# Performance work log

Measured on AMD Instinct MI355X. Metric: run time of the kernel, lower is better.

## Reference

```python
import jax, jax.numpy as jnp
import numpy as np

B_IN, C_OUT, K, P, STRIDE, ITERS = 32, 32, 3, 4, 2, 3
PSIZE = P * P
EPS = 1e-08
LAMBDA = 0.001
LN_2PI = float(np.log(2.0 * np.pi))


def _patch(t, K, stride):
    # t: (b, h, w, B, d) -> (b, oh, ow, K, K, B, d)
    b, h, w, B, d = t.shape
    oh = (h - K + 1) // stride
    idxs = jnp.arange(oh)[:, None] * stride + jnp.arange(K)[None, :]  # (oh, K)
    t = t[:, idxs]            # (b, oh, K, w, B, d)
    t = t[:, :, :, idxs]      # (b, oh, K, ow, K, B, d)
    t = jnp.transpose(t, (0, 1, 3, 2, 4, 5, 6))  # (b, oh, ow, K, K, B, d)
    return t, oh, oh


def _em_routing(v, a_in, beta_u, beta_a):
    # v: (b,h,w,Bn,C,psize); a_in: (b,h,w,Bn,1)
    b, h, w, Bn, C, psize = v.shape
    mu = sigma_sq = a_out = None
    for it in range(ITERS):
        if it == 0:
            r = jnp.full((b, h, w, Bn, C), 1.0 / C, dtype=v.dtype) * a_in
        else:
            ln_pjh = -((v - mu) ** 2) / (2.0 * sigma_sq) - 0.5 * jnp.log(sigma_sq) - 0.5 * LN_2PI
            ln_ap = ln_pjh.sum(axis=5) + jnp.log(a_out.reshape(b, h, w, 1, C))
            r = jax.nn.softmax(ln_ap, axis=4)
        r_sum = r.sum(axis=3, keepdims=True)                 # (b,h,w,1,C)
        coeff = (r / (r_sum + EPS))[..., None]               # (b,h,w,Bn,C,1)
        mu = jnp.sum(coeff * v, axis=3, keepdims=True)       # (b,h,w,1,C,psize)
        sigma_sq = jnp.sum(coeff * (v - mu) ** 2, axis=3, keepdims=True)
        r_sum6 = r_sum[..., None]                            # (b,h,w,1,C,1)
        cost_h = (beta_u + 0.5 * jnp.log(sigma_sq)) * r_sum6 # log(sqrt(s)) = 0.5*log(s)
        a_out = jax.nn.sigmoid(LAMBDA * (beta_a - cost_h.sum(axis=5, keepdims=True)))
    return mu.reshape(b, h, w, C, psize), a_out.reshape(b, h, w, C, 1)


def setup_inputs() -> dict:
    key = jax.random.key(0)
    k1, k2, k3 = jax.random.split(key, 3)
    b, h, w = 16, 14, 14
    x = jax.random.normal(k1, (b, h, w, B_IN, PSIZE), dtype=jnp.float32)
    a = jax.random.uniform(k2, (b, h, w, B_IN, 1), dtype=jnp.float32)
    weights = jax.random.normal(k3, (1, 1, 1, K * K * B_IN, C_OUT, P, P), dtype=jnp.float32)
    beta_u = jnp.zeros((C_OUT, 1), dtype=jnp.float32)
    beta_a = jnp.zeros((C_OUT, 1), dtype=jnp.float32)
    return {"x": x, "a": a, "weights": weights, "beta_u": beta_u, "beta_a": beta_a}


def reference(x, a, weights, beta_u, beta_a):
    b = x.shape[0]
    p_in, oh, ow = _patch(x, K, STRIDE)
    a_in, _, _ = _patch(a, K, STRIDE)
    KKB = K * K * B_IN
    p_in = p_in.reshape(b, oh, ow, KKB, PSIZE)
    a_in = a_in.reshape(b, oh, ow, KKB, 1)
    # voting: per-capsule PxP pose matmul with transformation matrices
    pose = p_in.reshape(b, oh, ow, KKB, P, P)
    W = weights.reshape(KKB, C_OUT, P, P)
    v = jnp.einsum('bhwnij,ncjl->bhwncil', pose, W).reshape(b, oh, ow, KKB, C_OUT, PSIZE)
    return _em_routing(v, a_in, beta_u, beta_a)
```

## Files before the change

### kernel.cpp

```cpp
#include <hip/hip_runtime.h>


#define LN2PI 1.8378770664093453f
#define LOG2E 1.4426950408889634f

typedef __attribute__((ext_vector_type(2))) float f32x2;
#define FMA2(a, b, c) __builtin_elementwise_fma((a), (b), (c))
__device__ __forceinline__ f32x2 splat2(float x) { f32x2 r; r.x = x; r.y = x; return r; }

#define DPP_ADD(x, ctrl) \
    ((x) + __int_as_float(__builtin_amdgcn_update_dpp( \
        0, __float_as_int(x), (ctrl), 0xF, 0xF, true)))

__device__ __forceinline__ float sum32(float e) {
    float s = e;
    s = DPP_ADD(s, 0xB1);
    s = DPP_ADD(s, 0x4E);
    s = DPP_ADD(s, 0x141);
    s = DPP_ADD(s, 0x140);
    s += __shfl_xor(s, 16);
    return s;
}

__global__ __launch_bounds__(256)
void wtrans(const float4* __restrict__ W4, float4* __restrict__ Wt)
{
    int idx = blockIdx.x * 256 + threadIdx.x;
    if (idx < 36864) {
        int n = idx >> 7;
        int r = idx & 127;
        int c = r >> 2, q = r & 3;
        Wt[((n * 4 + q) << 5) + c] = W4[idx];
    }
}

__global__ __launch_bounds__(256, 2)
void em_fused(const float* __restrict__ x,
              const float* __restrict__ a,
              const float4* __restrict__ Wt,
              const float* __restrict__ bu,
              const float* __restrict__ ba,
              float* __restrict__ out)
{
    __shared__ __align__(16) float4 pose_s[288 * 4];
    __shared__ float ain_s[288];
    __shared__ float SA[2][32][17];
    __shared__ float SB[2][32][17];
    __shared__ f32x2 php_s[32][9];
    __shared__ f32x2 mh_s[32][9];
    __shared__ float A_s[32];
    __shared__ float AU_s[32];

    const int tid  = threadIdx.x;
    const int wv   = tid >> 6;
    const int lane = tid & 63;
    const int half = (lane >> 5) & 1;
    const int c    = lane & 31;

    const int pos = blockIdx.x;
    const int b   = pos / 36;
    const int rem = pos % 36;
    const int oy  = rem / 6, ox = rem % 6;
    const int iy0 = oy * 2, ix0 = ox * 2;

    {
        const float4* x4 = (const float4*)x;
        for (int idx = tid; idx < 1152; idx += 256) {
            int seg = idx >> 7, u = idx & 127;
            int kh = seg / 3, kw = seg % 3;
            pose_s[idx] = x4[((b * 14 + iy0 + kh) * 14 + (ix0 + kw)) * 128 + u];
        }
        for (int idx = tid; idx < 288; idx += 256) {
            int seg = idx >> 5, bi = idx & 31;
            int kh = seg / 3, kw = seg % 3;
            ain_s[idx] = a[((b * 14 + iy0 + kh) * 14 + (ix0 + kw)) * 32 + bi] * 0.03125f;
        }
    }
    __syncthreads();

    const int n0 = wv * 72 + half;

    for (int it = 0; it < 3; ++it) {
        f32x2 ph[8], mh[8];
        float Ac = 0.f;
        if (it > 0) {
            #pragma unroll
            for (int j = 0; j < 8; ++j) { ph[j] = php_s[c][j]; mh[j] = mh_s[c][j]; }
            float AU = AU_s[c];
            float m = AU;
            #pragma unroll
            for (int mk = 16; mk >= 1; mk >>= 1)
                m = fmaxf(m, __shfl_xor(m, mk));
            Ac = A_s[c] - m;
        }

        f32x2 s1[8], s2[8];
        #pragma unroll
        for (int j = 0; j < 8; ++j) { s1[j] = splat2(0.f); s2[j] = splat2(0.f); }
        float Racc = 0.f;

        const float4* wp = Wt + (size_t)n0 * 128 + c;
        const float4* pp = pose_s + n0 * 4;
        const float* an  = ain_s + n0;

        for (int s = 0; s < 18; ++s) {
            float4 wa0 = wp[0],   wa1 = wp[32],  wa2 = wp[64],  wa3 = wp[96];
            float4 wb0 = wp[256], wb1 = wp[288], wb2 = wp[320], wb3 = wp[352];
            float4 pa0 = pp[0],  pa1 = pp[1],  pa2 = pp[2],  pa3 = pp[3];
            float4 pb0 = pp[8],  pb1 = pp[9],  pb2 = pp[10], pb3 = pp[11];

            f32x2 wa[8], wb[8];
            wa[0].x=wa0.x; wa[0].y=wa0.y;  wa[1].x=wa0.z; wa[1].y=wa0.w;
            wa[2].x=wa1.x; wa[2].y=wa1.y;  wa[3].x=wa1.z; wa[3].y=wa1.w;
            wa[4].x=wa2.x; wa[4].y=wa2.y;  wa[5].x=wa2.z; wa[5].y=wa2.w;
            wa[6].x=wa3.x; wa[6].y=wa3.y;  wa[7].x=wa3.z; wa[7].y=wa3.w;
            wb[0].x=wb0.x; wb[0].y=wb0.y;  wb[1].x=wb0.z; wb[1].y=wb0.w;
            wb[2].x=wb1.x; wb[2].y=wb1.y;  wb[3].x=wb1.z; wb[3].y=wb1.w;
            wb[4].x=wb2.x; wb[4].y=wb2.y;  wb[5].x=wb2.z; wb[5].y=wb2.w;
            wb[6].x=wb3.x; wb[6].y=wb3.y;  wb[7].x=wb3.z; wb[7].y=wb3.w;

            f32x2 va[8], vb[8];
            #pragma unroll
            for (int i = 0; i < 4; ++i) {
                float4 pra = (i == 0) ? pa0 : (i == 1) ? pa1 : (i == 2) ? pa2 : pa3;
                float4 prb = (i == 0) ? pb0 : (i == 1) ? pb1 : (i == 2) ? pb2 : pb3;
                #pragma unroll
                for (int lp = 0; lp < 2; ++lp) {
                    f32x2 ta = splat2(pra.x) * wa[0 + lp];
                    f32x2 tb = splat2(prb.x) * wb[0 + lp];
                    ta = FMA2(splat2(pra.y), wa[2 + lp], ta);
                    tb = FMA2(splat2(prb.y), wb[2 + lp], tb);
                    ta = FMA2(splat2(pra.z), wa[4 + lp], ta);
                    tb = FMA2(splat2(prb.z), wb[4 + lp], tb);
                    ta = FMA2(splat2(pra.w), wa[6 + lp], ta);
                    tb = FMA2(splat2(prb.w), wb[6 + lp], tb);
                    va[i * 2 + lp] = ta;
                    vb[i * 2 + lp] = tb;
                }
            }

            float ra, rb;
            if (it == 0) {
                ra = an[4 * s];
                rb = an[4 * s + 2];
            } else {
                f32x2 aa = splat2(0.f), ab = splat2(0.f);
                aa.x = Ac; ab.x = Ac;
                #pragma unroll
                for (int j = 0; j < 8; ++j) {
                    f32x2 ta = FMA2(ph[j], va[j], mh[j]);
                    f32x2 tb = FMA2(ph[j], vb[j], mh[j]);
                    aa = FMA2(ta, va[j], aa);
                    ab = FMA2(tb, vb[j], ab);
                }
                float ea = __builtin_amdgcn_exp2f(aa.x + aa.y);
                float eb = __builtin_amdgcn_exp2f(ab.x + ab.y);
                float sa = sum32(ea);
                float sb = sum32(eb);
                ra = __fdividef(ea, sa + 1e-30f);
                rb = __fdividef(eb, sb + 1e-30f);
            }

            Racc += ra + rb;
            f32x2 rra = splat2(ra), rrb = splat2(rb);
            #pragma unroll
            for (int j = 0; j < 8; ++j) {
                f32x2 rva = rra * va[j];
                f32x2 rvb = rrb * vb[j];
                s1[j] = s1[j] + rva + rvb;
                s2[j] = FMA2(rva, va[j], s2[j]);
                s2[j] = FMA2(rvb, vb[j], s2[j]);
            }

            wp += 512;
            pp += 16;
        }

        #pragma unroll
        for (int j = 0; j < 8; ++j) {
            s1[j].x += __shfl_xor(s1[j].x, 32);
            s1[j].y += __shfl_xor(s1[j].y, 32);
            s2[j].x += __shfl_xor(s2[j].x, 32);
            s2[j].y += __shfl_xor(s2[j].y, 32);
        }
        Racc += __shfl_xor(Racc, 32);

        if (wv >= 2) {
            const int row = wv - 2;
            if (half == 0) {
                #pragma unroll
                for (int j = 0; j < 8; ++j) {
                    SA[row][c][2 * j]     = s1[j].x;
                    SA[row][c][2 * j + 1] = s1[j].y;
                }
                SA[row][c][16] = Racc;
            } else {
                #pragma unroll
                for (int j = 0; j < 8; ++j) {
                    SB[row][c][2 * j]     = s2[j].x;
                    SB[row][c][2 * j + 1] = s2[j].y;
                }
            }
        }
        __syncthreads();
        if (wv < 2) {
            if (half == 0) {
                #pragma unroll
                for (int j = 0; j < 8; ++j) {
                    SA[wv][c][2 * j]     += s1[j].x;
                    SA[wv][c][2 * j + 1] += s1[j].y;
                }
                SA[wv][c][16] += Racc;
            } else {
                #pragma unroll
                for (int j = 0; j < 8; ++j) {
                    SB[wv][c][2 * j]     += s2[j].x;
                    SB[wv][c][2 * j + 1] += s2[j].y;
                }
            }
        }
        __syncthreads();

        {
            const int cf = tid >> 3, k2 = tid & 7;
            float R = SA[0][cf][16] + SA[1][cf][16];
            float rinv = __fdividef(1.f, R + 1e-8f);
            float muv[2];
            float tpart = 0.f, Ks = 0.f;
            #pragma unroll
            for (int t2 = 0; t2 < 2; ++t2) {
                int k = k2 + t2 * 8;
                float sv1 = SA[0][cf][k] + SA[1][cf][k];
                float sv2 = SB[0][cf][k] + SB[1][cf][k];
                float mu  = sv1 * rinv;
                float sig = fmaf(-mu, mu, sv2 * rinv);
                sig = fmaxf(sig, 1e-30f);
                float p = __fdividef(0.5f, sig);
                muv[t2] = mu;
                if (it < 2) {
                    ((float*)&php_s[cf][0])[k] = -p * LOG2E;
                    ((float*)&mh_s[cf][0])[k]  = 2.f * p * mu * LOG2E;
                }
                tpart += __logf(sig);
                Ks = fmaf(p * mu, mu, Ks);
            }
            #pragma unroll
            for (int mk = 4; mk >= 1; mk >>= 1) {
                tpart += __shfl_xor(tpart, mk);
                Ks    += __shfl_xor(Ks, mk);
            }
            float cost = R * fmaf(0.5f, tpart, 16.f * bu[cf]);
            float aout = __fdividef(1.f, 1.f + __expf(-(0.001f * (ba[cf] - cost))));

            if (it < 2) {
                if (k2 == 0) {
                    float Afold = __logf(aout) - 0.5f * tpart - 8.0f * LN2PI - Ks;
                    A_s[cf]  = Afold * LOG2E;
                    AU_s[cf] = (Afold + Ks) * LOG2E;
                }
            } else {
                out[(size_t)pos * 512 + cf * 16 + k2]     = muv[0];
                out[(size_t)pos * 512 + cf * 16 + k2 + 8] = muv[1];
                if (k2 == 0)
                    out[294912 + pos * 32 + cf] = aout;
            }
        }
        __syncthreads();
    }
}

#define NB 288
#define LNSTEP 36
__global__ __launch_bounds__(256, 2)
void convcaps_em_legacy(const float* __restrict__ x, const float* __restrict__ a,
                        const float* __restrict__ W, const float* __restrict__ bu,
                        const float* __restrict__ ba, float* __restrict__ out)
{
    __shared__ __align__(16) float pose_s[NB * 16];
    __shared__ __align__(16) float ain_s[NB];
    __shared__ float S1w[4][32][17];
    __shared__ float S2w[4][32][17];
    __shared__ float Rw[4][32];
    __shared__ float mu_s[32][17];
    __shared__ float p_s[32][17];
    __shared__ float A_s[32];

    const int tid = threadIdx.x, wv = tid >> 6, lane = tid & 63;
    const int half = (lane >> 5) & 1, c = lane & 31;
    const int bid = blockIdx.x, b = bid / 36, rem = bid % 36;
    const int oy = rem / 6, ox = rem % 6, iy0 = oy * 2, ix0 = ox * 2;
    {
        const float4* x4 = (const float4*)x;
        float4* d4 = (float4*)pose_s;
        for (int idx = tid; idx < 1152; idx += 256) {
            int seg = idx >> 7, u = idx & 127, kh = seg / 3, kw = seg % 3;
            d4[idx] = x4[((b * 14 + iy0 + kh) * 14 + (ix0 + kw)) * 128 + u];
        }
        const float4* a4 = (const float4*)a;
        float4* e4 = (float4*)ain_s;
        if (tid < 72) {
            int seg = tid >> 3, u = tid & 7, kh = seg / 3, kw = seg % 3;
            e4[tid] = a4[((b * 14 + iy0 + kh) * 14 + (ix0 + kw)) * 8 + u];
        }
    }
    __syncthreads();
    const float4* W4 = (const float4*)W;
    float muh[16], ph[16], Ac = 0.0f;
    #pragma unroll
    for (int i = 0; i < 16; ++i) { muh[i] = 0.0f; ph[i] = 0.0f; }
    for (int iter = 0; iter < 3; ++iter) {
        if (iter > 0) {
            #pragma unroll
            for (int il = 0; il < 16; ++il) { muh[il] = mu_s[c][il]; ph[il] = p_s[c][il]; }
            Ac = A_s[c];
        }
        float S1[16], S2[16], Racc = 0.0f;
        #pragma unroll
        for (int i = 0; i < 16; ++i) { S1[i] = 0.0f; S2[i] = 0.0f; }
        for (int s = 0; s < LNSTEP; ++s) {
            const int n = wv * 72 + 2 * s + half;
            float wreg[16], preg[16];
            const float4* wp = W4 + (size_t)(n * 32 + c) * 4;
            float4 w0 = wp[0], w1 = wp[1], w2 = wp[2], w3 = wp[3];
            wreg[0]=w0.x; wreg[1]=w0.y; wreg[2]=w0.z; wreg[3]=w0.w;
            wreg[4]=w1.x; wreg[5]=w1.y; wreg[6]=w1.z; wreg[7]=w1.w;
            wreg[8]=w2.x; wreg[9]=w2.y; wreg[10]=w2.z; wreg[11]=w2.w;
            wreg[12]=w3.x; wreg[13]=w3.y; wreg[14]=w3.z; wreg[15]=w3.w;
            const float4* pp = (const float4*)&pose_s[n * 16];
            float4 p0 = pp[0], p1 = pp[1], p2 = pp[2], p3 = pp[3];
            preg[0]=p0.x; preg[1]=p0.y; preg[2]=p0.z; preg[3]=p0.w;
            preg[4]=p1.x; preg[5]=p1.y; preg[6]=p1.z; preg[7]=p1.w;
            preg[8]=p2.x; preg[9]=p2.y; preg[10]=p2.z; preg[11]=p2.w;
            preg[12]=p3.x; preg[13]=p3.y; preg[14]=p3.z; preg[15]=p3.w;
            float v[16];
            #pragma unroll
            for (int i = 0; i < 4; ++i)
                #pragma unroll
                for (int l = 0; l < 4; ++l) {
                    float acc = preg[i*4+0] * wreg[l];
                    acc = fmaf(preg[i*4+1], wreg[4+l], acc);
                    acc = fmaf(preg[i*4+2], wreg[8+l], acc);
                    acc = fmaf(preg[i*4+3], wreg[12+l], acc);
                    v[i*4+l] = acc;
                }
            float r;
            if (iter == 0) r = ain_s[n] * 0.03125f;
            else {
                float acc = 0.0f;
                #pragma unroll
                for (int il = 0; il < 16; ++il) { float d = v[il]-muh[il]; acc = fmaf(-ph[il], d*d, acc); }
                float lnap = Ac + acc, m = lnap;
                #pragma unroll
                for (int mk = 16; mk >= 1; mk >>= 1) m = fmaxf(m, __shfl_xor(m, mk));
                float e = __expf(lnap - m), ssum = e;
                #pragma unroll
                for (int mk = 16; mk >= 1; mk >>= 1) ssum += __shfl_xor(ssum, mk);
                r = __fdividef(e, ssum);
            }
            Racc += r;
            #pragma unroll
            for (int il = 0; il < 16; ++il) { float rv = r * v[il]; S1[il] += rv; S2[il] = fmaf(rv, v[il], S2[il]); }
        }
        #pragma unroll
        for (int il = 0; il < 16; ++il) { S1[il] += __shfl_xor(S1[il], 32); S2[il] += __shfl_xor(S2[il], 32); }
        Racc += __shfl_xor(Racc, 32);
        if (half == 0) {
            #pragma unroll
            for (int il = 0; il < 16; ++il) { S1w[wv][c][il] = S1[il]; S2w[wv][c][il] = S2[il]; }
            Rw[wv][c] = Racc;
        }
        __syncthreads();
        {
            const int c2 = tid >> 3, k = tid & 7;
            float R = Rw[0][c2] + Rw[1][c2] + Rw[2][c2] + Rw[3][c2];
            float rinv = __fdividef(1.0f, R + 1e-8f);
            float muv[2], pv[2], tpart = 0.0f;
            #pragma unroll
            for (int t2 = 0; t2 < 2; ++t2) {
                int il = k + t2 * 8;
                float s1 = S1w[0][c2][il]+S1w[1][c2][il]+S1w[2][c2][il]+S1w[3][c2][il];
                float s2 = S2w[0][c2][il]+S2w[1][c2][il]+S2w[2][c2][il]+S2w[3][c2][il];
                float mu = s1 * rinv;
                float sig = fmaf(-mu, mu, s2 * rinv);
                sig = fmaxf(sig, 1e-30f);
                muv[t2] = mu; pv[t2] = __fdividef(0.5f, sig); tpart += __logf(sig);
            }
            #pragma unroll
            for (int mk = 4; mk >= 1; mk >>= 1) tpart += __shfl_xor(tpart, mk);
            float cost = R * fmaf(0.5f, tpart, 16.0f * bu[c2]);
            float aout = __fdividef(1.0f, 1.0f + __expf(-(0.001f * (ba[c2] - cost))));
            if (iter < 2) {
                #pragma unroll
                for (int t2 = 0; t2 < 2; ++t2) { int il = k + t2*8; mu_s[c2][il] = muv[t2]; p_s[c2][il] = pv[t2]; }
                if (k == 0) A_s[c2] = __logf(aout) - 0.5f * tpart - 8.0f * LN2PI;
            } else {
                #pragma unroll
                for (int t2 = 0; t2 < 2; ++t2) { int il = k + t2*8; out[(size_t)bid*512 + c2*16 + il] = muv[t2]; }
                if (k == 0) out[294912 + bid * 32 + c2] = aout;
            }
        }
        __syncthreads();
    }
}

extern "C" void kernel_launch(void* const* d_in, const int* in_sizes, int n_in,
                              void* d_out, int out_size, void* d_ws, size_t ws_size,
                              hipStream_t stream) {
    (void)in_sizes; (void)n_in; (void)out_size;
    const float* x  = (const float*)d_in[0];
    const float* a  = (const float*)d_in[1];
    const float* w  = (const float*)d_in[2];
    const float* bu = (const float*)d_in[3];
    const float* ba = (const float*)d_in[4];
    float* out = (float*)d_out;
    float* wsf = (float*)d_ws;

    if (ws_size >= (size_t)147456 * 4) {
        float* Wt = wsf;
        hipLaunchKernelGGL(wtrans, dim3(144), dim3(256), 0, stream,
                           (const float4*)w, (float4*)Wt);
        hipLaunchKernelGGL(em_fused, dim3(576), dim3(256), 0, stream,
                           x, a, (const float4*)Wt, bu, ba, out);
    } else {
        hipLaunchKernelGGL(convcaps_em_legacy, dim3(576), dim3(256), 0, stream,
                           x, a, w, bu, ba, out);
    }
}
```

Measured before the change: 92.76 us.

## Read pose directly from global memory and process one capsule per loop step

Drops the shared-memory staging of the pose patch. Each lane now loads its pose rows straight from global memory, with the address recomputed whenever the input capsule index crosses a 32-capsule segment. The inner loop handles one input capsule per iteration instead of two interleaved ones, and the occupancy hint is removed from launch_bounds. This removes the staging loads, the LDS traffic and part of the register pressure. In exchange the pose rows are re-read from global/L2 in every routing iteration and there is less instruction-level parallelism per loop step.

```diff
diff --git a/kernel.cpp b/kernel.cpp
--- a/kernel.cpp
+++ b/kernel.cpp
@@ -34,7 +34,7 @@
     }
 }
 
-__global__ __launch_bounds__(256, 2)
+__global__ __launch_bounds__(256)
 void em_fused(const float* __restrict__ x,
               const float* __restrict__ a,
               const float4* __restrict__ Wt,
@@ -42,7 +42,6 @@
               const float* __restrict__ ba,
               float* __restrict__ out)
 {
-    __shared__ __align__(16) float4 pose_s[288 * 4];
     __shared__ float ain_s[288];
     __shared__ float SA[2][32][17];
     __shared__ float SB[2][32][17];
@@ -63,18 +62,12 @@
     const int oy  = rem / 6, ox = rem % 6;
     const int iy0 = oy * 2, ix0 = ox * 2;
 
-    {
-        const float4* x4 = (const float4*)x;
-        for (int idx = tid; idx < 1152; idx += 256) {
-            int seg = idx >> 7, u = idx & 127;
-            int kh = seg / 3, kw = seg % 3;
-            pose_s[idx] = x4[((b * 14 + iy0 + kh) * 14 + (ix0 + kw)) * 128 + u];
-        }
-        for (int idx = tid; idx < 288; idx += 256) {
-            int seg = idx >> 5, bi = idx & 31;
-            int kh = seg / 3, kw = seg % 3;
-            ain_s[idx] = a[((b * 14 + iy0 + kh) * 14 + (ix0 + kw)) * 32 + bi] * 0.03125f;
-        }
+    const float4* x4 = (const float4*)x;
+
+    for (int idx = tid; idx < 288; idx += 256) {
+        int seg = idx >> 5, bi = idx & 31;
+        int kh = seg / 3, kw = seg % 3;
+        ain_s[idx] = a[((b * 14 + iy0 + kh) * 14 + (ix0 + kw)) * 32 + bi] * 0.03125f;
     }
     __syncthreads();
 
@@ -100,80 +93,76 @@
         float Racc = 0.f;
 
         const float4* wp = Wt + (size_t)n0 * 128 + c;
-        const float4* pp = pose_s + n0 * 4;
         const float* an  = ain_s + n0;
 
-        for (int s = 0; s < 18; ++s) {
-            float4 wa0 = wp[0],   wa1 = wp[32],  wa2 = wp[64],  wa3 = wp[96];
-            float4 wb0 = wp[256], wb1 = wp[288], wb2 = wp[320], wb3 = wp[352];
-            float4 pa0 = pp[0],  pa1 = pp[1],  pa2 = pp[2],  pa3 = pp[3];
-            float4 pb0 = pp[8],  pb1 = pp[9],  pb2 = pp[10], pb3 = pp[11];
-
-            f32x2 wa[8], wb[8];
-            wa[0].x=wa0.x; wa[0].y=wa0.y;  wa[1].x=wa0.z; wa[1].y=wa0.w;
-            wa[2].x=wa1.x; wa[2].y=wa1.y;  wa[3].x=wa1.z; wa[3].y=wa1.w;
-            wa[4].x=wa2.x; wa[4].y=wa2.y;  wa[5].x=wa2.z; wa[5].y=wa2.w;
-            wa[6].x=wa3.x; wa[6].y=wa3.y;  wa[7].x=wa3.z; wa[7].y=wa3.w;
-            wb[0].x=wb0.x; wb[0].y=wb0.y;  wb[1].x=wb0.z; wb[1].y=wb0.w;
-            wb[2].x=wb1.x; wb[2].y=wb1.y;  wb[3].x=wb1.z; wb[3].y=wb1.w;
-            wb[4].x=wb2.x; wb[4].y=wb2.y;  wb[5].x=wb2.z; wb[5].y=wb2.w;
-            wb[6].x=wb3.x; wb[6].y=wb3.y;  wb[7].x=wb3.z; wb[7].y=wb3.w;
-
-            f32x2 va[8], vb[8];
+        int n = n0;
+        const float4* px;
+        {
+            int seg = n >> 5, bi = n & 31;
+            int kh = (seg * 86) >> 8;
+            int kw = seg - 3 * kh;
+            px = x4 + ((size_t)((b * 14 + iy0 + kh) * 14 + (ix0 + kw)) * 32 + bi) * 4;
+        }
+
+        for (int s = 0; s < 36; ++s) {
+            float4 wr0 = wp[0], wr1 = wp[32], wr2 = wp[64], wr3 = wp[96];
+            float4 pr0 = px[0], pr1 = px[1], pr2 = px[2], pr3 = px[3];
+
+            f32x2 w2[8];
+            w2[0].x = wr0.x; w2[0].y = wr0.y;  w2[1].x = wr0.z; w2[1].y = wr0.w;
+            w2[2].x = wr1.x; w2[2].y = wr1.y;  w2[3].x = wr1.z; w2[3].y = wr1.w;
+            w2[4].x = wr2.x; w2[4].y = wr2.y;  w2[5].x = wr2.z; w2[5].y = wr2.w;
+            w2[6].x = wr3.x; w2[6].y = wr3.y;  w2[7].x = wr3.z; w2[7].y = wr3.w;
+
+            f32x2 v2[8];
             #pragma unroll
             for (int i = 0; i < 4; ++i) {
-                float4 pra = (i == 0) ? pa0 : (i == 1) ? pa1 : (i == 2) ? pa2 : pa3;
-                float4 prb = (i == 0) ? pb0 : (i == 1) ? pb1 : (i == 2) ? pb2 : pb3;
+                float4 pr = (i == 0) ? pr0 : (i == 1) ? pr1 : (i == 2) ? pr2 : pr3;
                 #pragma unroll
                 for (int lp = 0; lp < 2; ++lp) {
-                    f32x2 ta = splat2(pra.x) * wa[0 + lp];
-                    f32x2 tb = splat2(prb.x) * wb[0 + lp];
-                    ta = FMA2(splat2(pra.y), wa[2 + lp], ta);
-                    tb = FMA2(splat2(prb.y), wb[2 + lp], tb);
-                    ta = FMA2(splat2(pra.z), wa[4 + lp], ta);
-                    tb = FMA2(splat2(prb.z), wb[4 + lp], tb);
-                    ta = FMA2(splat2(pra.w), wa[6 + lp], ta);
-                    tb = FMA2(splat2(prb.w), wb[6 + lp], tb);
-                    va[i * 2 + lp] = ta;
-                    vb[i * 2 + lp] = tb;
-                }
-            }
-
-            float ra, rb;
+                    f32x2 t = splat2(pr.x) * w2[0 + lp];
+                    t = FMA2(splat2(pr.y), w2[2 + lp], t);
+                    t = FMA2(splat2(pr.z), w2[4 + lp], t);
+                    t = FMA2(splat2(pr.w), w2[6 + lp], t);
+                    v2[i * 2 + lp] = t;
+                }
+            }
+
+            float r;
             if (it == 0) {
-                ra = an[4 * s];
-                rb = an[4 * s + 2];
-            } else {
-                f32x2 aa = splat2(0.f), ab = splat2(0.f);
-                aa.x = Ac; ab.x = Ac;
+                r = an[2 * s];
+            } else {
+                f32x2 acc2 = splat2(0.f);
+                acc2.x = Ac;
                 #pragma unroll
                 for (int j = 0; j < 8; ++j) {
-                    f32x2 ta = FMA2(ph[j], va[j], mh[j]);
-                    f32x2 tb = FMA2(ph[j], vb[j], mh[j]);
-                    aa = FMA2(ta, va[j], aa);
-                    ab = FMA2(tb, vb[j], ab);
-                }
-                float ea = __builtin_amdgcn_exp2f(aa.x + aa.y);
-                float eb = __builtin_amdgcn_exp2f(ab.x + ab.y);
-                float sa = sum32(ea);
-                float sb = sum32(eb);
-                ra = __fdividef(ea, sa + 1e-30f);
-                rb = __fdividef(eb, sb + 1e-30f);
-            }
-
-            Racc += ra + rb;
-            f32x2 rra = splat2(ra), rrb = splat2(rb);
+                    f32x2 t = FMA2(ph[j], v2[j], mh[j]);
+                    acc2 = FMA2(t, v2[j], acc2);
+                }
+                float e = __builtin_amdgcn_exp2f(acc2.x + acc2.y);
+                float ssum = sum32(e);
+                r = __fdividef(e, ssum + 1e-30f);
+            }
+
+            Racc += r;
+            f32x2 rr = splat2(r);
             #pragma unroll
             for (int j = 0; j < 8; ++j) {
-                f32x2 rva = rra * va[j];
-                f32x2 rvb = rrb * vb[j];
-                s1[j] = s1[j] + rva + rvb;
-                s2[j] = FMA2(rva, va[j], s2[j]);
-                s2[j] = FMA2(rvb, vb[j], s2[j]);
-            }
-
-            wp += 512;
-            pp += 16;
+                f32x2 rv = rr * v2[j];
+                s1[j] = s1[j] + rv;
+                s2[j] = FMA2(rv, v2[j], s2[j]);
+            }
+
+            wp += 256;
+            n += 2;
+            if ((n & 31) < 2) {
+                int seg = n >> 5, bi = n & 31;
+                int kh = (seg * 86) >> 8;
+                int kw = seg - 3 * kh;
+                px = x4 + ((size_t)((b * 14 + iy0 + kh) * 14 + (ix0 + kw)) * 32 + bi) * 4;
+            } else {
+                px += 8;
+            }
         }
 
         #pragma unroll
```

Result: slower. 96.83 us (+4.4%).
